# Performance work log

Hardware: AMD Instinct MI355X
Metric: run time of the kernel (lower is better)

The kernel has to match this reference:

```python
import jax, jax.numpy as jnp
import numpy as np

N_NODES = 100000
N_EDGES = 1600000
IN_C, HID_C, OUT_C = 64, 64, 16


def _sage_conv(x, src, dst, W_l, b_l, W_r, num_nodes):
    # PyG SAGEConv (aggr='mean'): out = lin_l(mean_{j->i} x_j) + lin_r(x_i)
    # aggregate first (cheap small-d features), then one GEMM
    msg_sum = jax.ops.segment_sum(x[src], dst, num_segments=num_nodes)
    deg = jax.ops.segment_sum(jnp.ones_like(dst, dtype=x.dtype), dst,
                              num_segments=num_nodes)
    mean = msg_sum / jnp.maximum(deg, 1.0)[:, None]
    return mean @ W_l + b_l + x @ W_r


def setup_inputs() -> dict:
    key = jax.random.key(0)
    ks = jax.random.split(key, 8)
    x = jax.random.normal(ks[0], (N_NODES, IN_C), dtype=jnp.float32)
    edge_index = jax.random.randint(ks[1], (2, N_EDGES), 0, N_NODES, dtype=jnp.int64)
    # Glorot-ish init for weights; lin_l has bias, lin_r has none (PyG default)
    def glorot(k, fan_in, fan_out):
        s = jnp.sqrt(6.0 / (fan_in + fan_out))
        return jax.random.uniform(k, (fan_in, fan_out), jnp.float32, -s, s)
    return {
        "x": x,
        "edge_index": edge_index,
        "W1_l": glorot(ks[2], IN_C, HID_C),
        "b1": jnp.zeros((HID_C,), jnp.float32),
        "W1_r": glorot(ks[3], IN_C, HID_C),
        "W2_l": glorot(ks[4], HID_C, OUT_C),
        "b2": jnp.zeros((OUT_C,), jnp.float32),
        "W2_r": glorot(ks[5], HID_C, OUT_C),
    }


def reference(x, edge_index, W1_l, b1, W1_r, W2_l, b2, W2_r):
    src, dst = edge_index[0], edge_index[1]
    h = _sage_conv(x, src, dst, W1_l, b1, W1_r, N_NODES)
    h = jax.nn.relu(h)
    # dropout p=0.3 is identity in eval mode
    out = _sage_conv(h, src, dst, W2_l, b2, W2_r, N_NODES)
    return out
```

## Files before the change

### kernel.cpp

```cpp
#include <hip/hip_runtime.h>
#include <hip/hip_fp16.h>

#define N_NODES 100000
#define N_EDGES 1600000
#define IN_C 64
#define HID_C 64
#define OUT_C 16

#define BKT 256
#define BSH 8
#define NBKT 391
#define CAP 5120
#define GB 512
#define EPB 3125

typedef _Float16 f16x8 __attribute__((ext_vector_type(8)));
typedef float f32x16 __attribute__((ext_vector_type(16)));

__global__ __launch_bounds__(512) void k_bin(
    const int* __restrict__ src, const int* __restrict__ dst,
    int* __restrict__ gcnt, int* __restrict__ binned) {
  __shared__ int h[NBKT];
  __shared__ int cur[NBKT];
  int t = threadIdx.x;
  for (int i = t; i < NBKT; i += 512) h[i] = 0;
  __syncthreads();
  int base = blockIdx.x * EPB;
  int end = base + EPB;
  for (int e = base + t; e < end; e += 512)
    atomicAdd(&h[dst[e] >> BSH], 1);
  __syncthreads();
  for (int i = t; i < NBKT; i += 512) {
    int c = h[i];
    int b0 = atomicAdd(&gcnt[i], c);
    cur[i] = i * CAP + b0;
  }
  __syncthreads();
  for (int e = base + t; e < end; e += 512) {
    int d = dst[e];
    int pos = atomicAdd(&cur[d >> BSH], 1);
    binned[pos] = (src[e] << BSH) | (d & (BKT - 1));
  }
}

__global__ __launch_bounds__(512) void k_finalize(
    const int* __restrict__ binned, const int* __restrict__ gcnt,
    int* __restrict__ csr, int* __restrict__ rowstart, int* __restrict__ cnt) {
  int b = blockIdx.x;
  __shared__ int hcnt[BKT];
  __shared__ int hscan[BKT];
  __shared__ int cur[BKT];
  int t = threadIdx.x;
  if (t < BKT) hcnt[t] = 0;
  __syncthreads();
  int start = b * CAP;
  int end = start + gcnt[b];
  for (int i = start + t; i < end; i += 512)
    atomicAdd(&hcnt[binned[i] & (BKT - 1)], 1);
  __syncthreads();
  int v = 0;
  if (t < BKT) {
    v = hcnt[t];
    hscan[t] = v;
  }
  __syncthreads();
  for (int st = 1; st < 256; st <<= 1) {
    int a = 0;
    if (t < BKT && t >= st) a = hscan[t - st];
    __syncthreads();
    if (t < BKT) hscan[t] += a;
    __syncthreads();
  }
  if (t < BKT) {
    int rs = start + hscan[t] - v;
    cur[t] = rs;
    int n = (b << BSH) + t;
    if (n < N_NODES) {
      rowstart[n] = rs;
      cnt[n] = v;
    }
  }
  __syncthreads();
  for (int i = start + t; i < end; i += 512) {
    int vv = binned[i];
    int pos = atomicAdd(&cur[vv & (BKT - 1)], 1);
    csr[pos] = vv >> BSH;
  }
}

__global__ __launch_bounds__(256) void k_gemm1(
    const float* __restrict__ x, const float* __restrict__ Wl,
    const float* __restrict__ Wr, const float* __restrict__ b,
    __half* __restrict__ p, __half* __restrict__ q) {
  __shared__ _Float16 sA[64 * 68];
  __shared__ _Float16 sW[128 * 68];
  int t = threadIdx.x;
  int n0 = blockIdx.x * 64;

  for (int f = t; f < 1024; f += 256) {
    int r = f >> 4, c4 = f & 15;
    int n = n0 + r;
    float4 v = {0.0f, 0.0f, 0.0f, 0.0f};
    if (n < N_NODES) v = *(const float4*)&x[(size_t)n * 64 + c4 * 4];
    union { _Float16 h[4]; float2 f2; } u;
    u.h[0] = (_Float16)v.x; u.h[1] = (_Float16)v.y;
    u.h[2] = (_Float16)v.z; u.h[3] = (_Float16)v.w;
    *(float2*)&sA[r * 68 + c4 * 4] = u.f2;
  }
  for (int f = t; f < 2048; f += 256) {
    int k = f >> 5, c4 = f & 31;
    float4 w = (c4 < 16) ? *(const float4*)&Wl[k * 64 + c4 * 4]
                         : *(const float4*)&Wr[k * 64 + (c4 - 16) * 4];
    int c = c4 * 4;
    sW[(c + 0) * 68 + k] = (_Float16)w.x;
    sW[(c + 1) * 68 + k] = (_Float16)w.y;
    sW[(c + 2) * 68 + k] = (_Float16)w.z;
    sW[(c + 3) * 68 + k] = (_Float16)w.w;
  }
  __syncthreads();

  int w = t >> 6, lane = t & 63;
  int m = lane & 31, half = lane >> 5;
  int rt = w & 1, cg = w >> 1;

  f32x16 acc[2];
#pragma unroll
  for (int r = 0; r < 16; ++r) { acc[0][r] = 0.0f; acc[1][r] = 0.0f; }

  const _Float16* pA = &sA[(rt * 32 + m) * 68 + half * 8];
  const _Float16* pB0 = &sW[(cg * 64 + m) * 68 + half * 8];
  const _Float16* pB1 = &sW[(cg * 64 + 32 + m) * 68 + half * 8];
#pragma unroll
  for (int kc = 0; kc < 4; ++kc) {
    union { f16x8 v; float2 f2[2]; } a, b0, b1;
    a.f2[0] = *(const float2*)(pA + kc * 16);
    a.f2[1] = *(const float2*)(pA + kc * 16 + 4);
    b0.f2[0] = *(const float2*)(pB0 + kc * 16);
    b0.f2[1] = *(const float2*)(pB0 + kc * 16 + 4);
    b1.f2[0] = *(const float2*)(pB1 + kc * 16);
    b1.f2[1] = *(const float2*)(pB1 + kc * 16 + 4);
    acc[0] = __builtin_amdgcn_mfma_f32_32x32x16_f16(a.v, b0.v, acc[0], 0, 0, 0);
    acc[1] = __builtin_amdgcn_mfma_f32_32x32x16_f16(a.v, b1.v, acc[1], 0, 0, 0);
  }

  if (cg == 0) {
#pragma unroll
    for (int tt = 0; tt < 2; ++tt) {
      int col = tt * 32 + m;
#pragma unroll
      for (int r = 0; r < 16; ++r) {
        int row = (r & 3) + 4 * half + 8 * (r >> 2);
        int n = n0 + rt * 32 + row;
        if (n < N_NODES) p[(size_t)n * 64 + col] = __float2half(acc[tt][r]);
      }
    }
  } else {
    float bias[2] = {b[m], b[32 + m]};
#pragma unroll
    for (int tt = 0; tt < 2; ++tt) {
      int col = tt * 32 + m;
#pragma unroll
      for (int r = 0; r < 16; ++r) {
        int row = (r & 3) + 4 * half + 8 * (r >> 2);
        int n = n0 + rt * 32 + row;
        if (n < N_NODES)
          q[(size_t)n * 64 + col] = __float2half(acc[tt][r] + bias[tt]);
      }
    }
  }
}

__global__ __launch_bounds__(256) void k_fuse1(
    const float4* __restrict__ p1, const int* __restrict__ rowstart,
    const int* __restrict__ cnt, const int* __restrict__ csr,
    float4* __restrict__ q1h) {
  int t = threadIdx.x;
  int n = blockIdx.x * 32 + (t >> 3);
  int c4 = t & 7;
  int row = rowstart[n];
  int deg = cnt[n];
  float acc[8];
#pragma unroll
  for (int m = 0; m < 8; ++m) acc[m] = 0.0f;
  int j = 0;
  for (; j + 8 <= deg; j += 8) {
    int idx[8];
#pragma unroll
    for (int u = 0; u < 8; ++u) idx[u] = csr[row + j + u];
    float4 av[8];
#pragma unroll
    for (int u = 0; u < 8; ++u) av[u] = p1[idx[u] * 8 + c4];
#pragma unroll
    for (int u = 0; u < 8; ++u) {
      const __half2* h = (const __half2*)&av[u];
#pragma unroll
      for (int m = 0; m < 4; ++m) {
        float2 f = __half22float2(h[m]);
        acc[2 * m] += f.x;
        acc[2 * m + 1] += f.y;
      }
    }
  }
  for (; j + 4 <= deg; j += 4) {
    int idx[4];
#pragma unroll
    for (int u = 0; u < 4; ++u) idx[u] = csr[row + j + u];
    float4 av[4];
#pragma unroll
    for (int u = 0; u < 4; ++u) av[u] = p1[idx[u] * 8 + c4];
#pragma unroll
    for (int u = 0; u < 4; ++u) {
      const __half2* h = (const __half2*)&av[u];
#pragma unroll
      for (int m = 0; m < 4; ++m) {
        float2 f = __half22float2(h[m]);
        acc[2 * m] += f.x;
        acc[2 * m + 1] += f.y;
      }
    }
  }
  for (; j < deg; ++j) {
    float4 a = p1[csr[row + j] * 8 + c4];
    const __half2* h = (const __half2*)&a;
#pragma unroll
    for (int m = 0; m < 4; ++m) {
      float2 f = __half22float2(h[m]);
      acc[2 * m] += f.x;
      acc[2 * m + 1] += f.y;
    }
  }
  float inv = 1.0f / fmaxf((float)deg, 1.0f);
  int o = n * 8 + c4;
  float4 qv = q1h[o];
  __half2* qh = (__half2*)&qv;
  float4 r;
  __half2* rh = (__half2*)&r;
#pragma unroll
  for (int m = 0; m < 4; ++m) {
    float2 f = __half22float2(qh[m]);
    float2 s;
    s.x = fmaxf(acc[2 * m] * inv + f.x, 0.0f);
    s.y = fmaxf(acc[2 * m + 1] * inv + f.y, 0.0f);
    rh[m] = __float22half2_rn(s);
  }
  q1h[o] = r;
}

__global__ __launch_bounds__(256) void k_gemm2(
    const __half* __restrict__ h, const float* __restrict__ Wl,
    const float* __restrict__ Wr, const float* __restrict__ b,
    __half* __restrict__ p, float* __restrict__ q) {
  __shared__ _Float16 sA[128 * 68];
  __shared__ _Float16 sW[32 * 68];
  int t = threadIdx.x;
  int n0 = blockIdx.x * 128;

  for (int f = t; f < 2048; f += 256) {
    int r = f >> 4, c4 = f & 15;
    int n = n0 + r;
    float2 v = {0.0f, 0.0f};
    if (n < N_NODES) v = *(const float2*)&h[(size_t)n * 64 + c4 * 4];
    *(float2*)&sA[r * 68 + c4 * 4] = v;
  }
  for (int f = t; f < 512; f += 256) {
    int k = f >> 3, c4 = f & 7;
    float4 w = (c4 < 4) ? *(const float4*)&Wl[k * 16 + c4 * 4]
                        : *(const float4*)&Wr[k * 16 + (c4 - 4) * 4];
    int c = c4 * 4;
    sW[(c + 0) * 68 + k] = (_Float16)w.x;
    sW[(c + 1) * 68 + k] = (_Float16)w.y;
    sW[(c + 2) * 68 + k] = (_Float16)w.z;
    sW[(c + 3) * 68 + k] = (_Float16)w.w;
  }
  __syncthreads();

  int w = t >> 6, lane = t & 63;
  int m = lane & 31, half = lane >> 5;

  f32x16 acc;
#pragma unroll
  for (int r = 0; r < 16; ++r) acc[r] = 0.0f;

  const _Float16* pA = &sA[(w * 32 + m) * 68 + half * 8];
  const _Float16* pB = &sW[m * 68 + half * 8];
#pragma unroll
  for (int kc = 0; kc < 4; ++kc) {
    union { f16x8 v; float2 f2[2]; } a, bb;
    a.f2[0] = *(const float2*)(pA + kc * 16);
    a.f2[1] = *(const float2*)(pA + kc * 16 + 4);
    bb.f2[0] = *(const float2*)(pB + kc * 16);
    bb.f2[1] = *(const float2*)(pB + kc * 16 + 4);
    acc = __builtin_amdgcn_mfma_f32_32x32x16_f16(a.v, bb.v, acc, 0, 0, 0);
  }

  if (m < 16) {
#pragma unroll
    for (int r = 0; r < 16; ++r) {
      int row = (r & 3) + 4 * half + 8 * (r >> 2);
      int n = n0 + w * 32 + row;
      if (n < N_NODES) p[(size_t)n * 16 + m] = __float2half(acc[r]);
    }
  } else {
    float bias = b[m - 16];
#pragma unroll
    for (int r = 0; r < 16; ++r) {
      int row = (r & 3) + 4 * half + 8 * (r >> 2);
      int n = n0 + w * 32 + row;
      if (n < N_NODES) q[(size_t)n * 16 + (m - 16)] = acc[r] + bias;
    }
  }
}

__global__ __launch_bounds__(256) void k_fuse2(
    const float4* __restrict__ p2, const float4* __restrict__ q2,
    const int* __restrict__ rowstart, const int* __restrict__ cnt,
    const int* __restrict__ csr, float4* __restrict__ out) {
  int t = threadIdx.x;
  int n = blockIdx.x * 128 + (t >> 1);
  if (n >= N_NODES) return;
  int c8 = t & 1;
  int row = rowstart[n];
  int deg = cnt[n];
  float acc[8];
#pragma unroll
  for (int m = 0; m < 8; ++m) acc[m] = 0.0f;
  int j = 0;
  for (; j + 8 <= deg; j += 8) {
    int idx[8];
#pragma unroll
    for (int u = 0; u < 8; ++u) idx[u] = csr[row + j + u];
    float4 av[8];
#pragma unroll
    for (int u = 0; u < 8; ++u) av[u] = p2[idx[u] * 2 + c8];
#pragma unroll
    for (int u = 0; u < 8; ++u) {
      const __half2* h = (const __half2*)&av[u];
#pragma unroll
      for (int m = 0; m < 4; ++m) {
        float2 f = __half22float2(h[m]);
        acc[2 * m] += f.x;
        acc[2 * m + 1] += f.y;
      }
    }
  }
  for (; j < deg; ++j) {
    float4 a = p2[csr[row + j] * 2 + c8];
    const __half2* h = (const __half2*)&a;
#pragma unroll
    for (int m = 0; m < 4; ++m) {
      float2 f = __half22float2(h[m]);
      acc[2 * m] += f.x;
      acc[2 * m + 1] += f.y;
    }
  }
  float inv = 1.0f / fmaxf((float)deg, 1.0f);
  float4 q0 = q2[n * 4 + c8 * 2];
  float4 q1v = q2[n * 4 + c8 * 2 + 1];
  float4 o0 = {acc[0] * inv + q0.x, acc[1] * inv + q0.y,
               acc[2] * inv + q0.z, acc[3] * inv + q0.w};
  float4 o1 = {acc[4] * inv + q1v.x, acc[5] * inv + q1v.y,
               acc[6] * inv + q1v.z, acc[7] * inv + q1v.w};
  out[n * 4 + c8 * 2] = o0;
  out[n * 4 + c8 * 2 + 1] = o1;
}

extern "C" void kernel_launch(void* const* d_in, const int* in_sizes, int n_in,
                              void* d_out, int out_size, void* d_ws, size_t ws_size,
                              hipStream_t stream) {
  const float* x   = (const float*)d_in[0];
  const int* edge  = (const int*)d_in[1];
  const int* src   = edge;
  const int* dst   = edge + N_EDGES;
  const float* W1l = (const float*)d_in[2];
  const float* b1  = (const float*)d_in[3];
  const float* W1r = (const float*)d_in[4];
  const float* W2l = (const float*)d_in[5];
  const float* b2  = (const float*)d_in[6];
  const float* W2r = (const float*)d_in[7];
  float* out = (float*)d_out;

  int* gcnt     = (int*)d_ws;
  int* rowstart = gcnt + 512;
  int* cnt      = rowstart + N_NODES;
  int* binned   = cnt + N_NODES;
  int* csr      = binned + NBKT * CAP;
  __half* p1    = (__half*)(csr + NBKT * CAP);
  __half* q1h   = p1 + (size_t)N_NODES * 64;
  __half* p2    = p1;
  float* q2     = (float*)(p1 + (size_t)N_NODES * 16);

  hipMemsetAsync(gcnt, 0, NBKT * sizeof(int), stream);

  k_bin<<<GB, 512, 0, stream>>>(src, dst, gcnt, binned);
  k_finalize<<<NBKT, 512, 0, stream>>>(binned, gcnt, csr, rowstart, cnt);

  k_gemm1<<<(N_NODES + 63) / 64, 256, 0, stream>>>(x, W1l, W1r, b1, p1, q1h);
  k_fuse1<<<N_NODES / 32, 256, 0, stream>>>((const float4*)p1, rowstart, cnt,
                                            csr, (float4*)q1h);

  k_gemm2<<<(N_NODES + 127) / 128, 256, 0, stream>>>(q1h, W2l, W2r, b2, p2, q2);
  k_fuse2<<<(N_NODES + 127) / 128, 256, 0, stream>>>((const float4*)p2,
                                                     (const float4*)q2,
                                                     rowstart, cnt, csr,
                                                     (float4*)out);
}
```

Baseline: 202.5 us.

## Merge edge binning into GEMM1 launch and fuse CSR finalize with layer-1 aggregation

```diff
diff --git a/kernel.cpp b/kernel.cpp
--- a/kernel.cpp
+++ b/kernel.cpp
@@ -13,89 +13,46 @@
 #define CAP 5120
 #define GB 512
 #define EPB 3125
+#define G1B 1563
 
 typedef _Float16 f16x8 __attribute__((ext_vector_type(8)));
 typedef float f32x16 __attribute__((ext_vector_type(16)));
 
-__global__ __launch_bounds__(512) void k_bin(
+__global__ __launch_bounds__(256) void k_merged1(
     const int* __restrict__ src, const int* __restrict__ dst,
-    int* __restrict__ gcnt, int* __restrict__ binned) {
-  __shared__ int h[NBKT];
-  __shared__ int cur[NBKT];
-  int t = threadIdx.x;
-  for (int i = t; i < NBKT; i += 512) h[i] = 0;
-  __syncthreads();
-  int base = blockIdx.x * EPB;
-  int end = base + EPB;
-  for (int e = base + t; e < end; e += 512)
-    atomicAdd(&h[dst[e] >> BSH], 1);
-  __syncthreads();
-  for (int i = t; i < NBKT; i += 512) {
-    int c = h[i];
-    int b0 = atomicAdd(&gcnt[i], c);
-    cur[i] = i * CAP + b0;
-  }
-  __syncthreads();
-  for (int e = base + t; e < end; e += 512) {
-    int d = dst[e];
-    int pos = atomicAdd(&cur[d >> BSH], 1);
-    binned[pos] = (src[e] << BSH) | (d & (BKT - 1));
-  }
-}
-
-__global__ __launch_bounds__(512) void k_finalize(
-    const int* __restrict__ binned, const int* __restrict__ gcnt,
-    int* __restrict__ csr, int* __restrict__ rowstart, int* __restrict__ cnt) {
-  int b = blockIdx.x;
-  __shared__ int hcnt[BKT];
-  __shared__ int hscan[BKT];
-  __shared__ int cur[BKT];
-  int t = threadIdx.x;
-  if (t < BKT) hcnt[t] = 0;
-  __syncthreads();
-  int start = b * CAP;
-  int end = start + gcnt[b];
-  for (int i = start + t; i < end; i += 512)
-    atomicAdd(&hcnt[binned[i] & (BKT - 1)], 1);
-  __syncthreads();
-  int v = 0;
-  if (t < BKT) {
-    v = hcnt[t];
-    hscan[t] = v;
-  }
-  __syncthreads();
-  for (int st = 1; st < 256; st <<= 1) {
-    int a = 0;
-    if (t < BKT && t >= st) a = hscan[t - st];
-    __syncthreads();
-    if (t < BKT) hscan[t] += a;
-    __syncthreads();
-  }
-  if (t < BKT) {
-    int rs = start + hscan[t] - v;
-    cur[t] = rs;
-    int n = (b << BSH) + t;
-    if (n < N_NODES) {
-      rowstart[n] = rs;
-      cnt[n] = v;
-    }
-  }
-  __syncthreads();
-  for (int i = start + t; i < end; i += 512) {
-    int vv = binned[i];
-    int pos = atomicAdd(&cur[vv & (BKT - 1)], 1);
-    csr[pos] = vv >> BSH;
-  }
-}
-
-__global__ __launch_bounds__(256) void k_gemm1(
+    int* __restrict__ gcnt, int* __restrict__ binned,
     const float* __restrict__ x, const float* __restrict__ Wl,
     const float* __restrict__ Wr, const float* __restrict__ b,
     __half* __restrict__ p, __half* __restrict__ q) {
   __shared__ _Float16 sA[64 * 68];
   __shared__ _Float16 sW[128 * 68];
   int t = threadIdx.x;
-  int n0 = blockIdx.x * 64;
+
+  if (blockIdx.x < GB) {
+    int* h   = (int*)sA;
+    int* cur = (int*)sW;
+    for (int i = t; i < NBKT; i += 256) h[i] = 0;
+    __syncthreads();
+    int base = blockIdx.x * EPB;
+    int end = base + EPB;
+    for (int e = base + t; e < end; e += 256)
+      atomicAdd(&h[dst[e] >> BSH], 1);
+    __syncthreads();
+    for (int i = t; i < NBKT; i += 256) {
+      int c = h[i];
+      int b0 = atomicAdd(&gcnt[i], c);
+      cur[i] = i * CAP + b0;
+    }
+    __syncthreads();
+    for (int e = base + t; e < end; e += 256) {
+      int d = dst[e];
+      int pos = atomicAdd(&cur[d >> BSH], 1);
+      binned[pos] = (src[e] << BSH) | (d & (BKT - 1));
+    }
+    return;
+  }
+
+  int n0 = (blockIdx.x - GB) * 64;
 
   for (int f = t; f < 1024; f += 256) {
     int r = f >> 4, c4 = f & 15;
@@ -170,29 +127,85 @@
   }
 }
 
-__global__ __launch_bounds__(256) void k_fuse1(
-    const float4* __restrict__ p1, const int* __restrict__ rowstart,
-    const int* __restrict__ cnt, const int* __restrict__ csr,
+__global__ __launch_bounds__(512) void k_fuse1b(
+    const float4* __restrict__ p1, const int* __restrict__ gcnt,
+    const int* __restrict__ binned, int* __restrict__ csr,
+    int* __restrict__ rowstart, int* __restrict__ cnt,
     float4* __restrict__ q1h) {
+  __shared__ int hcnt[BKT];
+  __shared__ int hscan[BKT];
+  __shared__ int cur[BKT];
+  __shared__ int lcsr[CAP];
+  int b = blockIdx.x;
   int t = threadIdx.x;
-  int n = blockIdx.x * 32 + (t >> 3);
-  int c4 = t & 7;
-  int row = rowstart[n];
-  int deg = cnt[n];
-  float acc[8];
-#pragma unroll
-  for (int m = 0; m < 8; ++m) acc[m] = 0.0f;
-  int j = 0;
-  for (; j + 8 <= deg; j += 8) {
-    int idx[8];
-#pragma unroll
-    for (int u = 0; u < 8; ++u) idx[u] = csr[row + j + u];
-    float4 av[8];
-#pragma unroll
-    for (int u = 0; u < 8; ++u) av[u] = p1[idx[u] * 8 + c4];
-#pragma unroll
-    for (int u = 0; u < 8; ++u) {
-      const __half2* h = (const __half2*)&av[u];
+  if (t < BKT) hcnt[t] = 0;
+  __syncthreads();
+  int start = b * CAP;
+  int total = gcnt[b];
+  for (int i = t; i < total; i += 512)
+    atomicAdd(&hcnt[binned[start + i] & (BKT - 1)], 1);
+  __syncthreads();
+  int v = 0;
+  if (t < BKT) {
+    v = hcnt[t];
+    hscan[t] = v;
+  }
+  __syncthreads();
+  for (int st = 1; st < 256; st <<= 1) {
+    int a = 0;
+    if (t < BKT && t >= st) a = hscan[t - st];
+    __syncthreads();
+    if (t < BKT) hscan[t] += a;
+    __syncthreads();
+  }
+  if (t < BKT) {
+    cur[t] = hscan[t] - v;
+    int n = (b << BSH) + t;
+    if (n < N_NODES) {
+      rowstart[n] = start + hscan[t] - v;
+      cnt[n] = v;
+    }
+  }
+  __syncthreads();
+  for (int i = t; i < total; i += 512) {
+    int vv = binned[start + i];
+    int pos = atomicAdd(&cur[vv & (BKT - 1)], 1);
+    lcsr[pos] = vv >> BSH;
+  }
+  __syncthreads();
+  for (int i = t; i < total; i += 512) csr[start + i] = lcsr[i];
+
+  int g = t >> 3, c4 = t & 7;
+  for (int r = g; r < BKT; r += 64) {
+    int n = (b << BSH) + r;
+    if (n >= N_NODES) continue;
+    int deg = hcnt[r];
+    int row = hscan[r] - deg;
+    float acc[8];
+#pragma unroll
+    for (int m = 0; m < 8; ++m) acc[m] = 0.0f;
+    int j = 0;
+    for (; j + 8 <= deg; j += 8) {
+      int idx[8];
+#pragma unroll
+      for (int u = 0; u < 8; ++u) idx[u] = lcsr[row + j + u];
+      float4 av[8];
+#pragma unroll
+      for (int u = 0; u < 8; ++u) av[u] = p1[idx[u] * 8 + c4];
+#pragma unroll
+      for (int u = 0; u < 8; ++u) {
+        const __half2* h = (const __half2*)&av[u];
+#pragma unroll
+        for (int m = 0; m < 4; ++m) {
+          float2 f = __half22float2(h[m]);
+          acc[2 * m] += f.x;
+          acc[2 * m + 1] += f.y;
+        }
+      }
+    }
+    for (; j < deg; ++j) {
+      float4 a = p1[lcsr[row + j] * 8 + c4];
+      const __half2* h = (const __half2*)&a;
 #pragma unroll
       for (int m = 0; m < 4; ++m) {
         float2 f = __half22float2(h[m]);
@@ -200,50 +213,22 @@
         acc[2 * m + 1] += f.y;
       }
     }
-  }
-  for (; j + 4 <= deg; j += 4) {
-    int idx[4];
-#pragma unroll
-    for (int u = 0; u < 4; ++u) idx[u] = csr[row + j + u];
-    float4 av[4];
-#pragma unroll
-    for (int u = 0; u < 4; ++u) av[u] = p1[idx[u] * 8 + c4];
-#pragma unroll
-    for (int u = 0; u < 4; ++u) {
-      const __half2* h = (const __half2*)&av[u];
-#pragma unroll
-      for (int m = 0; m < 4; ++m) {
-        float2 f = __half22float2(h[m]);
-        acc[2 * m] += f.x;
-        acc[2 * m + 1] += f.y;
-      }
-    }
-  }
-  for (; j < deg; ++j) {
-    float4 a = p1[csr[row + j] * 8 + c4];
-    const __half2* h = (const __half2*)&a;
+    float inv = 1.0f / fmaxf((float)deg, 1.0f);
+    int o = n * 8 + c4;
+    float4 qv = q1h[o];
+    __half2* qh = (__half2*)&qv;
+    float4 res;
+    __half2* rh = (__half2*)&res;
 #pragma unroll
     for (int m = 0; m < 4; ++m) {
-      float2 f = __half22float2(h[m]);
-      acc[2 * m] += f.x;
-      acc[2 * m + 1] += f.y;
-    }
-  }
-  float inv = 1.0f / fmaxf((float)deg, 1.0f);
-  int o = n * 8 + c4;
-  float4 qv = q1h[o];
-  __half2* qh = (__half2*)&qv;
-  float4 r;
-  __half2* rh = (__half2*)&r;
-#pragma unroll
-  for (int m = 0; m < 4; ++m) {
-    float2 f = __half22float2(qh[m]);
-    float2 s;
-    s.x = fmaxf(acc[2 * m] * inv + f.x, 0.0f);
-    s.y = fmaxf(acc[2 * m + 1] * inv + f.y, 0.0f);
-    rh[m] = __float22half2_rn(s);
-  }
-  q1h[o] = r;
+      float2 f = __half22float2(qh[m]);
+      float2 s;
+      s.x = fmaxf(acc[2 * m] * inv + f.x, 0.0f);
+      s.y = fmaxf(acc[2 * m + 1] * inv + f.y, 0.0f);
+      rh[m] = __float22half2_rn(s);
+    }
+    q1h[o] = res;
+  }
 }
 
 __global__ __launch_bounds__(256) void k_gemm2(
@@ -391,13 +376,10 @@
 
   hipMemsetAsync(gcnt, 0, NBKT * sizeof(int), stream);
 
-  k_bin<<<GB, 512, 0, stream>>>(src, dst, gcnt, binned);
-  k_finalize<<<NBKT, 512, 0, stream>>>(binned, gcnt, csr, rowstart, cnt);
-
-  k_gemm1<<<(N_NODES + 63) / 64, 256, 0, stream>>>(x, W1l, W1r, b1, p1, q1h);
-  k_fuse1<<<N_NODES / 32, 256, 0, stream>>>((const float4*)p1, rowstart, cnt,
-                                            csr, (float4*)q1h);
-
+  k_merged1<<<GB + G1B, 256, 0, stream>>>(src, dst, gcnt, binned,
+                                          x, W1l, W1r, b1, p1, q1h);
+  k_fuse1b<<<NBKT, 512, 0, stream>>>((const float4*)p1, gcnt, binned, csr,
+                                     rowstart, cnt, (float4*)q1h);
   k_gemm2<<<(N_NODES + 127) / 128, 256, 0, stream>>>(q1h, W2l, W2r, b2, p2, q2);
   k_fuse2<<<(N_NODES + 127) / 128, 256, 0, stream>>>((const float4*)p2,
                                                      (const float4*)q2,
```

After: 193.0 us. -4.6%, faster.
